# Kernel tuning notes

Hardware: AMD Instinct MI355X
Metric: run time of the kernel (lower is better)

## Reference

```python
import jax, jax.numpy as jnp
import numpy as np

ATTN, ENC, DEC = 1024, 1024, 1024
B, S = 64, 2048

def setup_inputs() -> dict:
    key = jax.random.key(0)
    k1, k2, k3, k4, k5, k6 = jax.random.split(key, 6)
    sc_w = 1.0 / np.sqrt(ENC + DEC)
    sc_v = 1.0 / np.sqrt(ATTN)
    return {
        "hidden": jax.random.normal(k1, (B, DEC), dtype=jnp.float32),
        "vectors_to_attend": jax.random.normal(k2, (S, B, ENC), dtype=jnp.float32),
        "attn_w_weight": jax.random.uniform(k3, (ATTN, ENC + DEC), jnp.float32, -sc_w, sc_w),
        "attn_w_bias": jax.random.uniform(k4, (ATTN,), jnp.float32, -sc_w, sc_w),
        "attn_v_weight": jax.random.uniform(k5, (1, ATTN), jnp.float32, -sc_v, sc_v),
        "attn_v_bias": jax.random.uniform(k6, (1,), jnp.float32, -sc_v, sc_v),
    }

def reference(hidden, vectors_to_attend, attn_w_weight, attn_w_bias, attn_v_weight, attn_v_bias):
    # vectors_to_attend: [S, B, E] -> [B, S, E]
    v = jnp.transpose(vectors_to_attend, (1, 0, 2))
    # Split attn_w over the concat dim: concat([v, h]) @ W^T == v @ We^T + h @ Wd^T
    We = attn_w_weight[:, :ENC]   # [A, E]
    Wd = attn_w_weight[:, ENC:]   # [A, D]
    # energies: [B, S, A]
    e = jnp.tanh(jnp.einsum('bse,ae->bsa', v, We)
                 + jnp.einsum('bd,ad->ba', hidden, Wd)[:, None, :]
                 + attn_w_bias)
    # scores: [B, S]
    scores = jnp.einsum('bsa,a->bs', e, attn_v_weight[0]) + attn_v_bias[0]
    weights = jax.nn.softmax(scores, axis=1)          # softmax over seq dim
    context = jnp.einsum('bs,bse->be', weights, v)    # [B, E]
    return context[:, None, :]                        # [B, 1, E] to match bmm output
```

## Files before the change

kernel.cpp:

```cpp
#include <hip/hip_runtime.h>
#include <hip/hip_bf16.h>
#include <math.h>

#define BB 64
#define SS 2048
#define MT (SS*BB)
#define NSTEP 16

typedef __attribute__((ext_vector_type(4))) float f4;
typedef __attribute__((ext_vector_type(4))) int   i4;

__device__ __forceinline__ float fast_tanh(float x) {
  float t = __expf(2.0f * x);
  return 1.0f - 2.0f * __builtin_amdgcn_rcpf(t + 1.0f);
}

#define GLD16(gp, lp) __builtin_amdgcn_global_load_lds( \
    (const __attribute__((address_space(1))) void*)(gp), \
    (__attribute__((address_space(3))) void*)(lp), 16, 0, 0)
#define WAITV0() asm volatile("s_waitcnt vmcnt(0)" ::: "memory")
#define BAR()    __builtin_amdgcn_s_barrier()
#define SCHED0() __builtin_amdgcn_sched_barrier(0)

__global__ void k_packq(const float* __restrict__ src, unsigned char* __restrict__ dst,
                        int stride) {
  __shared__ float ls[64][260];
  int g = blockIdx.x, cb = blockIdx.y, tid = threadIdx.x;
  int cl = (tid & 63) * 4, rbk = tid >> 6;
  const float* s0 = src + (size_t)(g * 64) * stride + cb * 256 + cl;
  #pragma unroll
  for (int it = 0; it < 16; ++it) {
    int rr = it * 4 + rbk;
    *(f4*)&ls[rr][cl] = *(const f4*)(s0 + (size_t)rr * stride);
  }
  __syncthreads();
  int rr = tid & 63;
  int q = tid >> 6;
  int kt = cb * 2 + (q >> 1);
  int grow = g * 64 + rr;
  int panel = grow >> 8, pr = grow & 255, h = pr >> 7, r = pr & 127;
  int rx = r & 7;
  unsigned char* ub = dst + (((size_t)(panel * 8 + kt) * 2 + h) * 128 + r) * 128;
  #pragma unroll
  for (int si = 0; si < 4; ++si) {
    int s = (q & 1) * 4 + si;
    int sp = s ^ rx;
    const float* fp = &ls[rr][q * 64 + si * 16];
    i4 w;
    #pragma unroll
    for (int k = 0; k < 4; ++k) {
      int b = 0;
      b = __builtin_amdgcn_cvt_pk_fp8_f32(fp[k * 4 + 0], fp[k * 4 + 1], b, 0);
      b = __builtin_amdgcn_cvt_pk_fp8_f32(fp[k * 4 + 2], fp[k * 4 + 3], b, 1);
      w[k] = b;
    }
    *(i4*)(ub + sp * 16) = w;
  }
}

__global__ void k_hp(const float* __restrict__ hidden, const float* __restrict__ w,
                     const float* __restrict__ wbias, float* __restrict__ hp) {
  __shared__ float hs[1024];
  int b = blockIdx.x, tid = threadIdx.x;
  for (int i = tid; i < 1024; i += 256) hs[i] = hidden[b * 1024 + i];
  __syncthreads();
  int a = blockIdx.y * 256 + tid;
  const f4* wd = (const f4*)(w + a * 2048 + 1024);
  const f4* hv = (const f4*)hs;
  float acc = wbias[a];
  #pragma unroll 8
  for (int d = 0; d < 256; ++d) {
    f4 x = wd[d], y = hv[d];
    acc += x[0]*y[0] + x[1]*y[1] + x[2]*y[2] + x[3]*y[3];
  }
  hp[b * 1024 + a] = acc;
}

__global__ __launch_bounds__(512, 4) void k_gemm(
    const unsigned char* __restrict__ Aq, const unsigned char* __restrict__ Wq,
    const float* __restrict__ hp, const float* __restrict__ vw,
    float* __restrict__ part, int bm0, int nbm) {
  extern __shared__ char smem[];
  int bid = blockIdx.x;
  int nwg = nbm * 8;
  int cpx = nwg >> 3;
  int wg = (bid & 7) * cpx + (bid >> 3);
  int bn = wg & 7;
  int bmL = wg >> 3;
  int tid = threadIdx.x, lane = tid & 63;
  int wid = tid >> 6, wr = wid >> 1, wc = wid & 1;
  int c = lane & 15, kq = lane >> 4;

  int sxf0 = ((((kq >> 1)    ) ^ (c & 3)) << 4) + ((kq & 1) << 3);
  int sxf1 = ((((kq >> 1) + 2) ^ (c & 3)) << 4) + ((kq & 1) << 3);
  int aoff = (wr * 64 + c) * 64;
  int boff = 16384 + (wc * 64 + c) * 64;

  int rA = tid >> 2, jA = tid & 3;
  int jsw = jA ^ (rA & 3);
  int aco0 = (((jsw    ) ^ (rA & 7)) << 4);
  int aco1 = (((jsw + 4) ^ (rA & 7)) << 4);
  const unsigned char* aU = Aq + (size_t)bmL * 262144 + rA * 128;
  const unsigned char* bU = Wq + (size_t)(bn >> 1) * 262144 + (bn & 1) * 16384 + rA * 128;

  auto stage = [&](int tt) {
    int kt = tt >> 1;
    int co = (tt & 1) ? aco1 : aco0;
    char* dst = smem + (tt & 1) * 24576 + tid * 16;
    const unsigned char* as_ = aU + kt * 32768 + co;
    const unsigned char* bs_ = bU + kt * 32768 + co;
    GLD16(as_, dst);
    GLD16(as_ + 16384, dst + 8192);
    GLD16(bs_, dst + 16384);
  };

  f4 acc[4][4];
  f4 z = {0.f, 0.f, 0.f, 0.f};
  #pragma unroll
  for (int i = 0; i < 4; ++i)
    #pragma unroll
    for (int j = 0; j < 4; ++j) acc[i][j] = z;

#define MMK(SX) { \
    const char* ap_ = rb + aoff + (SX); \
    const char* bp_ = rb + boff + (SX); \
    long a0_ = *(const long*)(ap_);        long a1_ = *(const long*)(ap_ + 1024); \
    long a2_ = *(const long*)(ap_ + 2048); long a3_ = *(const long*)(ap_ + 3072); \
    long b0_ = *(const long*)(bp_);        long b1_ = *(const long*)(bp_ + 1024); \
    long b2_ = *(const long*)(bp_ + 2048); long b3_ = *(const long*)(bp_ + 3072); \
    __builtin_amdgcn_s_setprio(1); \
    acc[0][0] = __builtin_amdgcn_mfma_f32_16x16x32_fp8_fp8(a0_, b0_, acc[0][0], 0, 0, 0); \
    acc[0][1] = __builtin_amdgcn_mfma_f32_16x16x32_fp8_fp8(a0_, b1_, acc[0][1], 0, 0, 0); \
    acc[0][2] = __builtin_amdgcn_mfma_f32_16x16x32_fp8_fp8(a0_, b2_, acc[0][2], 0, 0, 0); \
    acc[0][3] = __builtin_amdgcn_mfma_f32_16x16x32_fp8_fp8(a0_, b3_, acc[0][3], 0, 0, 0); \
    acc[1][0] = __builtin_amdgcn_mfma_f32_16x16x32_fp8_fp8(a1_, b0_, acc[1][0], 0, 0, 0); \
    acc[1][1] = __builtin_amdgcn_mfma_f32_16x16x32_fp8_fp8(a1_, b1_, acc[1][1], 0, 0, 0); \
    acc[1][2] = __builtin_amdgcn_mfma_f32_16x16x32_fp8_fp8(a1_, b2_, acc[1][2], 0, 0, 0); \
    acc[1][3] = __builtin_amdgcn_mfma_f32_16x16x32_fp8_fp8(a1_, b3_, acc[1][3], 0, 0, 0); \
    acc[2][0] = __builtin_amdgcn_mfma_f32_16x16x32_fp8_fp8(a2_, b0_, acc[2][0], 0, 0, 0); \
    acc[2][1] = __builtin_amdgcn_mfma_f32_16x16x32_fp8_fp8(a2_, b1_, acc[2][1], 0, 0, 0); \
    acc[2][2] = __builtin_amdgcn_mfma_f32_16x16x32_fp8_fp8(a2_, b2_, acc[2][2], 0, 0, 0); \
    acc[2][3] = __builtin_amdgcn_mfma_f32_16x16x32_fp8_fp8(a2_, b3_, acc[2][3], 0, 0, 0); \
    acc[3][0] = __builtin_amdgcn_mfma_f32_16x16x32_fp8_fp8(a3_, b0_, acc[3][0], 0, 0, 0); \
    acc[3][1] = __builtin_amdgcn_mfma_f32_16x16x32_fp8_fp8(a3_, b1_, acc[3][1], 0, 0, 0); \
    acc[3][2] = __builtin_amdgcn_mfma_f32_16x16x32_fp8_fp8(a3_, b2_, acc[3][2], 0, 0, 0); \
    acc[3][3] = __builtin_amdgcn_mfma_f32_16x16x32_fp8_fp8(a3_, b3_, acc[3][3], 0, 0, 0); \
    __builtin_amdgcn_s_setprio(0); }

  stage(0);
  WAITV0();
  SCHED0(); BAR(); SCHED0();

  #pragma unroll 1
  for (int t = 0; t < NSTEP; ++t) {
    const char* rb = smem + (t & 1) * 24576;
    if (t < NSTEP - 1) stage(t + 1);
    MMK(sxf0);
    MMK(sxf1);
    if (t < NSTEP - 1) {
      WAITV0();
      SCHED0(); BAR(); SCHED0();
    }
  }
#undef MMK

  __syncthreads();
  {
    const float* hprow = hp + bn * 128;
    float* lhp = (float*)smem;
    #pragma unroll
    for (int qd = 0; qd < 4; ++qd) {
      int i = qd * 512 + tid;
      int b = i >> 5, col4 = i & 31;
      *(f4*)(lhp + b * 128 + col4 * 4) = *(const f4*)(hprow + (size_t)b * 1024 + col4 * 4);
    }
  }
  __syncthreads();
  const float* lhpf = (const float*)smem;

  int lg = kq;
  int bm = bm0 + bmL;
  float rs[4][4];
  #pragma unroll
  for (int mi = 0; mi < 4; ++mi)
    #pragma unroll
    for (int j = 0; j < 4; ++j) rs[mi][j] = 0.f;
  #pragma unroll
  for (int ni = 0; ni < 4; ++ni) {
    int colL = wc * 64 + ni * 16 + c;
    float vwa = vw[bn * 128 + colL];
    #pragma unroll
    for (int mi = 0; mi < 4; ++mi) {
      #pragma unroll
      for (int j = 0; j < 4; ++j) {
        int r = wr * 64 + mi * 16 + lg * 4 + j;
        int b = r & 63;
        float x = acc[mi][ni][j] + lhpf[b * 128 + colL];
        rs[mi][j] += fast_tanh(x) * vwa;
      }
    }
  }
  #pragma unroll
  for (int off = 1; off < 16; off <<= 1) {
    #pragma unroll
    for (int mi = 0; mi < 4; ++mi)
      #pragma unroll
      for (int j = 0; j < 4; ++j)
        rs[mi][j] += __shfl_xor(rs[mi][j], off, 64);
  }
  if (c == 0) {
    int p = bn * 2 + wc;
    #pragma unroll
    for (int mi = 0; mi < 4; ++mi)
      #pragma unroll
      for (int j = 0; j < 4; ++j) {
        int m = bm * 256 + wr * 64 + mi * 16 + lg * 4 + j;
        int b = m & 63, s = m >> 6;
        part[(size_t)p * MT + b * SS + s] = rs[mi][j];
      }
  }
}

__global__ void k_softmax(const float* __restrict__ part, float* __restrict__ wt) {
  int b = blockIdx.x, tid = threadIdx.x, lane = tid & 63, wid = tid >> 6;
  __shared__ float red[8];
  float sc[8];
  float mx = -1e30f;
  #pragma unroll
  for (int i = 0; i < 8; ++i) {
    int s = tid + i * 256;
    float a = 0.f;
    #pragma unroll
    for (int p = 0; p < 16; ++p) a += part[(size_t)p * MT + b * SS + s];
    sc[i] = a; mx = fmaxf(mx, a);
  }
  for (int o = 1; o < 64; o <<= 1) mx = fmaxf(mx, __shfl_xor(mx, o, 64));
  if (lane == 0) red[wid] = mx;
  __syncthreads();
  mx = fmaxf(fmaxf(red[0], red[1]), fmaxf(red[2], red[3]));
  float sum = 0.f;
  #pragma unroll
  for (int i = 0; i < 8; ++i) { sc[i] = expf(sc[i] - mx); sum += sc[i]; }
  for (int o = 1; o < 64; o <<= 1) sum += __shfl_xor(sum, o, 64);
  if (lane == 0) red[4 + wid] = sum;
  __syncthreads();
  sum = red[4] + red[5] + red[6] + red[7];
  float inv = 1.f / sum;
  #pragma unroll
  for (int i = 0; i < 8; ++i) wt[b * SS + tid + i * 256] = sc[i] * inv;
}

__global__ void k_ctx_f32(const float* __restrict__ v, const float* __restrict__ wt,
                          float* __restrict__ ctxp) {
  int b = blockIdx.x, cch = blockIdx.y, tid = threadIdx.x;
  f4 acc = {0.f, 0.f, 0.f, 0.f};
  int s0 = cch * 128;
  const float* wrow = wt + b * SS;
  #pragma unroll 4
  for (int s = s0; s < s0 + 128; ++s) {
    float ws = wrow[s];
    const f4* vp = (const f4*)(v + (size_t)(s * 64 + b) * 1024);
    acc += vp[tid] * ws;
  }
  *(f4*)(ctxp + (size_t)(cch * 64 + b) * 1024 + tid * 4) = acc;
}

__global__ void k_out(const float* __restrict__ ctxp, float* __restrict__ out) {
  int b = blockIdx.x, tid = threadIdx.x;
  f4 acc = {0.f, 0.f, 0.f, 0.f};
  #pragma unroll
  for (int cch = 0; cch < 16; ++cch)
    acc += *(const f4*)(ctxp + (size_t)(cch * 64 + b) * 1024 + tid * 4);
  *(f4*)(out + b * 1024 + tid * 4) = acc;
}

extern "C" void kernel_launch(void* const* d_in, const int* in_sizes, int n_in,
                              void* d_out, int out_size, void* d_ws, size_t ws_size,
                              hipStream_t stream) {
  const float* hidden = (const float*)d_in[0];
  const float* v      = (const float*)d_in[1];
  const float* ww     = (const float*)d_in[2];
  const float* wbias  = (const float*)d_in[3];
  const float* vwgt   = (const float*)d_in[4];
  float* out = (float*)d_out;

  char* ws = (char*)d_ws;
  float*          hp   = (float*)(ws);
  unsigned char*  wq   = (unsigned char*)(ws + 262144);
  float*          part = (float*)(ws + 262144 + 1048576);
  float*          wt   = (float*)(ws + 262144 + 1048576 + 8388608);
  float*          ctxp = (float*)(ws + 262144 + 1048576 + 8388608 + 524288);
  size_t fixed = 262144 + 1048576 + 8388608 + 524288 + 4194304;
  unsigned char*  vq   = (unsigned char*)(ws + fixed);

  size_t avail = (ws_size > fixed) ? (ws_size - fixed) : 0;
  long rows_chunk = (long)(avail / 1024) & ~511L;
  if (rows_chunk > MT) rows_chunk = MT;
  if (rows_chunk < 512) rows_chunk = 512;

  hipFuncSetAttribute((const void*)k_gemm, hipFuncAttributeMaxDynamicSharedMemorySize, 49152);

  k_packq<<<dim3(16, 4), 256, 0, stream>>>(ww, wq, 2048);
  k_hp<<<dim3(64, 4), 256, 0, stream>>>(hidden, ww, wbias, hp);

  for (long r0 = 0; r0 < MT; r0 += rows_chunk) {
    long nr = MT - r0; if (nr > rows_chunk) nr = rows_chunk;
    int nbm = (int)(nr / 256);
    k_packq<<<dim3((int)(nr / 64), 4), 256, 0, stream>>>(v + (size_t)r0 * 1024, vq, 1024);
    k_gemm<<<nbm * 8, 512, 49152, stream>>>(vq, wq, hp, vwgt, part, (int)(r0 / 256), nbm);
  }

  k_softmax<<<64, 256, 0, stream>>>(part, wt);
  k_ctx_f32<<<dim3(64, 16), 256, 0, stream>>>(v, wt, ctxp);
  k_out<<<64, 256, 0, stream>>>(ctxp, out);
}
```

Baseline: 580.6 us.

## Switch GEMM to 16x16x128 scaled FP8 MFMA with 128x128 tiles

Replaces the 16x16x32 fp8 MFMA inner loop with the MI355 scaled 16x16x128 f8f6f4 MFMA at unit scale, using 128-byte K slices per stage and half as many pipeline steps. The block tile changes from 256x128 to 128x128, with 2x4 waves, which doubles the number of workgroups and the partial-score slices (32 instead of 16). Softmax must now reduce twice as many partials, and the partial buffer and LDS size grow. The aim is higher MFMA throughput and fewer loop iterations, at the cost of less A-tile reuse per block and more partial-sum traffic.

```diff
diff --git a/kernel.cpp b/kernel.cpp
--- a/kernel.cpp
+++ b/kernel.cpp
@@ -5,14 +5,20 @@
 #define BB 64
 #define SS 2048
 #define MT (SS*BB)
-#define NSTEP 16
+#define NSTEP 8
 
 typedef __attribute__((ext_vector_type(4))) float f4;
 typedef __attribute__((ext_vector_type(4))) int   i4;
+typedef __attribute__((ext_vector_type(8))) int   i8;
 
 __device__ __forceinline__ float fast_tanh(float x) {
   float t = __expf(2.0f * x);
   return 1.0f - 2.0f * __builtin_amdgcn_rcpf(t + 1.0f);
+}
+
+__device__ __forceinline__ f4 mmq(i8 a, i8 b, f4 c) {
+  return __builtin_amdgcn_mfma_scale_f32_16x16x128_f8f6f4(
+      a, b, c, 0, 0, 0, 0x7F7F7F7F, 0, 0x7F7F7F7F);
 }
 
 #define GLD16(gp, lp) __builtin_amdgcn_global_load_lds( \
@@ -88,64 +94,37 @@
   int bn = wg & 7;
   int bmL = wg >> 3;
   int tid = threadIdx.x, lane = tid & 63;
-  int wid = tid >> 6, wr = wid >> 1, wc = wid & 1;
+  int wid = tid >> 6, wr = wid >> 2, wc = wid & 3;
   int c = lane & 15, kq = lane >> 4;
 
-  int sxf0 = ((((kq >> 1)    ) ^ (c & 3)) << 4) + ((kq & 1) << 3);
-  int sxf1 = ((((kq >> 1) + 2) ^ (c & 3)) << 4) + ((kq & 1) << 3);
-  int aoff = (wr * 64 + c) * 64;
-  int boff = 16384 + (wc * 64 + c) * 64;
-
-  int rA = tid >> 2, jA = tid & 3;
-  int jsw = jA ^ (rA & 3);
-  int aco0 = (((jsw    ) ^ (rA & 7)) << 4);
-  int aco1 = (((jsw + 4) ^ (rA & 7)) << 4);
-  const unsigned char* aU = Aq + (size_t)bmL * 262144 + rA * 128;
-  const unsigned char* bU = Wq + (size_t)(bn >> 1) * 262144 + (bn & 1) * 16384 + rA * 128;
-
-  auto stage = [&](int tt) {
-    int kt = tt >> 1;
-    int co = (tt & 1) ? aco1 : aco0;
-    char* dst = smem + (tt & 1) * 24576 + tid * 16;
-    const unsigned char* as_ = aU + kt * 32768 + co;
-    const unsigned char* bs_ = bU + kt * 32768 + co;
-    GLD16(as_, dst);
-    GLD16(as_ + 16384, dst + 8192);
-    GLD16(bs_, dst + 16384);
+  int sx0 = ((2 * kq) ^ (c & 7)) << 4;
+  int sx1 = sx0 ^ 16;
+  int aoff = (wr * 64 + c) * 128;
+  int boff = 16384 + (wc * 32 + c) * 128;
+
+  const unsigned char* aS0 = Aq + (size_t)(bmL >> 1) * 262144 + (bmL & 1) * 16384 + tid * 16;
+  const unsigned char* bS0 = Wq + (size_t)(bn >> 1) * 262144 + (bn & 1) * 16384 + tid * 16;
+  auto stage = [&](int kt) {
+    char* d = smem + (kt & 1) * 32768 + tid * 16;
+    const unsigned char* as_ = aS0 + (size_t)kt * 32768;
+    const unsigned char* bs_ = bS0 + (size_t)kt * 32768;
+    GLD16(as_, d);
+    GLD16(as_ + 8192, d + 8192);
+    GLD16(bs_, d + 16384);
+    GLD16(bs_ + 8192, d + 24576);
   };
 
-  f4 acc[4][4];
+  f4 acc[4][2];
   f4 z = {0.f, 0.f, 0.f, 0.f};
   #pragma unroll
-  for (int i = 0; i < 4; ++i)
-    #pragma unroll
-    for (int j = 0; j < 4; ++j) acc[i][j] = z;
-
-#define MMK(SX) { \
-    const char* ap_ = rb + aoff + (SX); \
-    const char* bp_ = rb + boff + (SX); \
-    long a0_ = *(const long*)(ap_);        long a1_ = *(const long*)(ap_ + 1024); \
-    long a2_ = *(const long*)(ap_ + 2048); long a3_ = *(const long*)(ap_ + 3072); \
-    long b0_ = *(const long*)(bp_);        long b1_ = *(const long*)(bp_ + 1024); \
-    long b2_ = *(const long*)(bp_ + 2048); long b3_ = *(const long*)(bp_ + 3072); \
-    __builtin_amdgcn_s_setprio(1); \
-    acc[0][0] = __builtin_amdgcn_mfma_f32_16x16x32_fp8_fp8(a0_, b0_, acc[0][0], 0, 0, 0); \
-    acc[0][1] = __builtin_amdgcn_mfma_f32_16x16x32_fp8_fp8(a0_, b1_, acc[0][1], 0, 0, 0); \
-    acc[0][2] = __builtin_amdgcn_mfma_f32_16x16x32_fp8_fp8(a0_, b2_, acc[0][2], 0, 0, 0); \
-    acc[0][3] = __builtin_amdgcn_mfma_f32_16x16x32_fp8_fp8(a0_, b3_, acc[0][3], 0, 0, 0); \
-    acc[1][0] = __builtin_amdgcn_mfma_f32_16x16x32_fp8_fp8(a1_, b0_, acc[1][0], 0, 0, 0); \
-    acc[1][1] = __builtin_amdgcn_mfma_f32_16x16x32_fp8_fp8(a1_, b1_, acc[1][1], 0, 0, 0); \
-    acc[1][2] = __builtin_amdgcn_mfma_f32_16x16x32_fp8_fp8(a1_, b2_, acc[1][2], 0, 0, 0); \
-    acc[1][3] = __builtin_amdgcn_mfma_f32_16x16x32_fp8_fp8(a1_, b3_, acc[1][3], 0, 0, 0); \
-    acc[2][0] = __builtin_amdgcn_mfma_f32_16x16x32_fp8_fp8(a2_, b0_, acc[2][0], 0, 0, 0); \
-    acc[2][1] = __builtin_amdgcn_mfma_f32_16x16x32_fp8_fp8(a2_, b1_, acc[2][1], 0, 0, 0); \
-    acc[2][2] = __builtin_amdgcn_mfma_f32_16x16x32_fp8_fp8(a2_, b2_, acc[2][2], 0, 0, 0); \
-    acc[2][3] = __builtin_amdgcn_mfma_f32_16x16x32_fp8_fp8(a2_, b3_, acc[2][3], 0, 0, 0); \
-    acc[3][0] = __builtin_amdgcn_mfma_f32_16x16x32_fp8_fp8(a3_, b0_, acc[3][0], 0, 0, 0); \
-    acc[3][1] = __builtin_amdgcn_mfma_f32_16x16x32_fp8_fp8(a3_, b1_, acc[3][1], 0, 0, 0); \
-    acc[3][2] = __builtin_amdgcn_mfma_f32_16x16x32_fp8_fp8(a3_, b2_, acc[3][2], 0, 0, 0); \
-    acc[3][3] = __builtin_amdgcn_mfma_f32_16x16x32_fp8_fp8(a3_, b3_, acc[3][3], 0, 0, 0); \
-    __builtin_amdgcn_s_setprio(0); }
+  for (int i = 0; i < 4; ++i) { acc[i][0] = z; acc[i][1] = z; }
+
+  i8 a0, a1, a2, a3, b0, b1;
+
+#define LD2(DST, ADDR) { \
+    i4 lo_ = *(const i4*)((ADDR) + sx0); \
+    i4 hi_ = *(const i4*)((ADDR) + sx1); \
+    DST = __builtin_shufflevector(lo_, hi_, 0, 1, 2, 3, 4, 5, 6, 7); }
 
   stage(0);
   WAITV0();
@@ -153,16 +132,24 @@
 
   #pragma unroll 1
   for (int t = 0; t < NSTEP; ++t) {
-    const char* rb = smem + (t & 1) * 24576;
+    const char* rb = smem + (t & 1) * 32768;
     if (t < NSTEP - 1) stage(t + 1);
-    MMK(sxf0);
-    MMK(sxf1);
+    const char* ap = rb + aoff;
+    const char* bp = rb + boff;
+    LD2(a0, ap);  LD2(a1, ap + 2048);  LD2(a2, ap + 4096);  LD2(a3, ap + 6144);
+    LD2(b0, bp);  LD2(b1, bp + 2048);
+    __builtin_amdgcn_s_setprio(1);
+    acc[0][0] = mmq(a0, b0, acc[0][0]);  acc[0][1] = mmq(a0, b1, acc[0][1]);
+    acc[1][0] = mmq(a1, b0, acc[1][0]);  acc[1][1] = mmq(a1, b1, acc[1][1]);
+    acc[2][0] = mmq(a2, b0, acc[2][0]);  acc[2][1] = mmq(a2, b1, acc[2][1]);
+    acc[3][0] = mmq(a3, b0, acc[3][0]);  acc[3][1] = mmq(a3, b1, acc[3][1]);
+    __builtin_amdgcn_s_setprio(0);
     if (t < NSTEP - 1) {
       WAITV0();
       SCHED0(); BAR(); SCHED0();
     }
   }
-#undef MMK
+#undef LD2
 
   __syncthreads();
   {
@@ -186,8 +173,8 @@
     #pragma unroll
     for (int j = 0; j < 4; ++j) rs[mi][j] = 0.f;
   #pragma unroll
-  for (int ni = 0; ni < 4; ++ni) {
-    int colL = wc * 64 + ni * 16 + c;
+  for (int ni = 0; ni < 2; ++ni) {
+    int colL = wc * 32 + ni * 16 + c;
     float vwa = vw[bn * 128 + colL];
     #pragma unroll
     for (int mi = 0; mi < 4; ++mi) {
@@ -209,12 +196,12 @@
         rs[mi][j] += __shfl_xor(rs[mi][j], off, 64);
   }
   if (c == 0) {
-    int p = bn * 2 + wc;
+    int p = bn * 4 + wc;
     #pragma unroll
     for (int mi = 0; mi < 4; ++mi)
       #pragma unroll
       for (int j = 0; j < 4; ++j) {
-        int m = bm * 256 + wr * 64 + mi * 16 + lg * 4 + j;
+        int m = bm * 128 + wr * 64 + mi * 16 + lg * 4 + j;
         int b = m & 63, s = m >> 6;
         part[(size_t)p * MT + b * SS + s] = rs[mi][j];
       }
@@ -231,7 +218,7 @@
     int s = tid + i * 256;
     float a = 0.f;
     #pragma unroll
-    for (int p = 0; p < 16; ++p) a += part[(size_t)p * MT + b * SS + s];
+    for (int p = 0; p < 32; ++p) a += part[(size_t)p * MT + b * SS + s];
     sc[i] = a; mx = fmaxf(mx, a);
   }
   for (int o = 1; o < 64; o <<= 1) mx = fmaxf(mx, __shfl_xor(mx, o, 64));
@@ -288,9 +275,9 @@
   float*          hp   = (float*)(ws);
   unsigned char*  wq   = (unsigned char*)(ws + 262144);
   float*          part = (float*)(ws + 262144 + 1048576);
-  float*          wt   = (float*)(ws + 262144 + 1048576 + 8388608);
-  float*          ctxp = (float*)(ws + 262144 + 1048576 + 8388608 + 524288);
-  size_t fixed = 262144 + 1048576 + 8388608 + 524288 + 4194304;
+  float*          wt   = (float*)(ws + 262144 + 1048576 + 16777216);
+  float*          ctxp = (float*)(ws + 262144 + 1048576 + 16777216 + 524288);
+  size_t fixed = 262144 + 1048576 + 16777216 + 524288 + 4194304;
   unsigned char*  vq   = (unsigned char*)(ws + fixed);
 
   size_t avail = (ws_size > fixed) ? (ws_size - fixed) : 0;
@@ -298,16 +285,16 @@
   if (rows_chunk > MT) rows_chunk = MT;
   if (rows_chunk < 512) rows_chunk = 512;
 
-  hipFuncSetAttribute((const void*)k_gemm, hipFuncAttributeMaxDynamicSharedMemorySize, 49152);
+  hipFuncSetAttribute((const void*)k_gemm, hipFuncAttributeMaxDynamicSharedMemorySize, 65536);
 
   k_packq<<<dim3(16, 4), 256, 0, stream>>>(ww, wq, 2048);
   k_hp<<<dim3(64, 4), 256, 0, stream>>>(hidden, ww, wbias, hp);
 
   for (long r0 = 0; r0 < MT; r0 += rows_chunk) {
     long nr = MT - r0; if (nr > rows_chunk) nr = rows_chunk;
-    int nbm = (int)(nr / 256);
+    int nbm = (int)(nr / 128);
     k_packq<<<dim3((int)(nr / 64), 4), 256, 0, stream>>>(v + (size_t)r0 * 1024, vq, 1024);
-    k_gemm<<<nbm * 8, 512, 49152, stream>>>(vq, wq, hp, vwgt, part, (int)(r0 / 256), nbm);
+    k_gemm<<<nbm * 8, 512, 65536, stream>>>(vq, wq, hp, vwgt, part, (int)(r0 / 128), nbm);
   }
 
   k_softmax<<<64, 256, 0, stream>>>(part, wt);
```

Result: faster. 516.6 us (-11.0%).
